# Kernel tuning notes

Hardware: AMD Instinct MI355X
Metric: run time of the kernel (lower is better)

The kernel has to match this reference:

```python
import jax, jax.numpy as jnp
import numpy as np

D_MODEL = 1024
NUM_HEADS = 16
ROPE_THETA = 10000.0
NEG_INF = -1.0e9  # matches torch masked_fill value


def _rope(x, cos, sin):
    # x: (B, H, S, d_k); cos/sin: (1, 1, S, d_k) with interleaved-pair layout
    x_even = x[..., ::2]
    x_odd = x[..., 1::2]
    x_rot = jnp.stack((-x_odd, x_even), axis=-1).reshape(x.shape)
    return x * cos + x_rot * sin


def setup_inputs() -> dict:
    key = jax.random.key(0)
    ks = jax.random.split(key, 5)
    B, S, D = 2, 2048, D_MODEL
    std = np.sqrt(2.0 / (D + D))
    return {
        "x": jax.random.normal(ks[0], (B, S, D), dtype=jnp.float32),
        "token_positions": jnp.arange(S, dtype=jnp.int32)[None, :],
        "Wq": jax.random.normal(ks[1], (D, D), dtype=jnp.float32) * std,
        "Wk": jax.random.normal(ks[2], (D, D), dtype=jnp.float32) * std,
        "Wv": jax.random.normal(ks[3], (D, D), dtype=jnp.float32) * std,
        "Wo": jax.random.normal(ks[4], (D, D), dtype=jnp.float32) * std,
    }


def reference(x, token_positions, Wq, Wk, Wv, Wo):
    B, S, D = x.shape
    H = NUM_HEADS
    dk = D // H

    def proj(W):
        return (x @ W.T).reshape(B, S, H, dk).transpose(0, 2, 1, 3)  # (B,H,S,dk)

    q, k, v = proj(Wq), proj(Wk), proj(Wv)

    # RoPE tables (interleaved repeat of each frequency)
    inv_freq = 1.0 / ROPE_THETA ** (jnp.arange(0, dk, 2, dtype=jnp.float32) / dk)
    angles = token_positions.astype(jnp.float32)[..., None] * inv_freq  # (1,S,dk/2)
    angles = jnp.repeat(angles, 2, axis=-1)  # (1,S,dk)
    cos = jnp.cos(angles)[:, None, :, :]  # (1,1,S,dk)
    sin = jnp.sin(angles)[:, None, :, :]
    q = _rope(q, cos, sin)
    k = _rope(k, cos, sin)

    scores = jnp.einsum("bhqd,bhkd->bhqk", q, k) / jnp.sqrt(jnp.float32(dk))
    causal = jnp.tril(jnp.ones((S, S), dtype=bool))
    scores = jnp.where(causal, scores, NEG_INF)
    attn = jax.nn.softmax(scores, axis=-1)
    out = jnp.einsum("bhqk,bhkd->bhqd", attn, v)
    out = out.transpose(0, 2, 1, 3).reshape(B, S, D)
    return out @ Wo.T
```

## Files before the change

kernel.cpp:

```cpp
#include <hip/hip_runtime.h>
#include <hip/hip_bf16.h>
#include <stdint.h>

typedef __bf16 bf16_t;
typedef __attribute__((ext_vector_type(8))) __bf16 bf16x8;
typedef __attribute__((ext_vector_type(4))) __bf16 bf16x4;
typedef __attribute__((ext_vector_type(2))) __bf16 bf16x2;
typedef __attribute__((ext_vector_type(4))) float f32x4;
typedef __attribute__((ext_vector_type(16))) float f32x16;
typedef __attribute__((ext_vector_type(4))) uint32_t u32x4;

#define S_LEN 2048
#define DMODEL 1024
#define NHEAD 16
#define DK 64
#define TENS_ELEMS 4194304

__device__ __forceinline__ void async_load16(const bf16_t* g, bf16_t* l) {
  __builtin_amdgcn_global_load_lds(
      (const __attribute__((address_space(1))) uint32_t*)(const void*)g,
      (__attribute__((address_space(3))) uint32_t*)(void*)l,
      16, 0, 0);
}

__device__ __forceinline__ uint32_t pack_bf16(float a, float b) {
  bf16x2 h; h[0] = (bf16_t)a; h[1] = (bf16_t)b;
  return __builtin_bit_cast(uint32_t, h);
}

__global__ __launch_bounds__(256) void cvt_all(const float* __restrict__ x,
                                               const float* __restrict__ w0,
                                               const float* __restrict__ w1,
                                               const float* __restrict__ w2,
                                               const float* __restrict__ w3,
                                               bf16_t* __restrict__ xb,
                                               bf16_t* __restrict__ wb) {
  int b = blockIdx.x;
  const float* s;
  bf16_t* d;
  int i;
  if (b < 4096) {
    s = x; d = xb; i = b * 256 + threadIdx.x;
  } else {
    int k = (b - 4096) >> 10, j = (b - 4096) & 1023;
    s = (k == 0) ? w0 : (k == 1) ? w1 : (k == 2) ? w2 : w3;
    d = wb + (size_t)k * 1048576;
    i = j * 256 + threadIdx.x;
  }
  float4 v = ((const float4*)s)[i];
  bf16x4 o;
  o.x = (bf16_t)v.x; o.y = (bf16_t)v.y; o.z = (bf16_t)v.z; o.w = (bf16_t)v.w;
  ((bf16x4*)d)[i] = o;
}

template <int MODE>
__global__ __launch_bounds__(256) void gemm_nt(const bf16_t* __restrict__ A,
                                               const bf16_t* __restrict__ Bw,
                                               bf16_t* __restrict__ Cb,
                                               float* __restrict__ Cf,
                                               const int* __restrict__ tok) {
  __shared__ bf16_t As[64 * 64];
  __shared__ bf16_t Bs[128 * 64];
  const int K = 1024;
  int tid = threadIdx.x;
  int lane = tid & 63, w = tid >> 6, lo = lane & 15, hi = lane >> 4;
  int m0 = blockIdx.y * 64, n0 = blockIdx.x * 128;
  const bf16_t* Bp = Bw + (size_t)blockIdx.z * 1048576;
  f32x4 acc[4][2] = {};
  for (int k0 = 0; k0 < K; k0 += 64) {
#pragma unroll
    for (int it = 0; it < 2; ++it) {
      int idx = it * 256 + tid;
      int row = idx >> 3, kc = (idx & 7) * 8;
      async_load16(A + (size_t)(m0 + row) * K + k0 + kc, &As[idx * 8]);
    }
#pragma unroll
    for (int it = 0; it < 4; ++it) {
      int idx = it * 256 + tid;
      int row = idx >> 3, kc = (idx & 7) * 8;
      async_load16(Bp + (size_t)(n0 + row) * K + k0 + kc, &Bs[idx * 8]);
    }
    __syncthreads();
#pragma unroll
    for (int ks = 0; ks < 2; ++ks) {
      bf16x8 af[4], bfr[2];
#pragma unroll
      for (int mi = 0; mi < 4; ++mi)
        af[mi] = *(const bf16x8*)&As[(mi * 16 + lo) * 64 + ks * 32 + hi * 8];
#pragma unroll
      for (int ni = 0; ni < 2; ++ni)
        bfr[ni] = *(const bf16x8*)&Bs[(w * 32 + ni * 16 + lo) * 64 + ks * 32 + hi * 8];
#pragma unroll
      for (int mi = 0; mi < 4; ++mi)
#pragma unroll
        for (int ni = 0; ni < 2; ++ni)
          acc[mi][ni] = __builtin_amdgcn_mfma_f32_16x16x32_bf16(af[mi], bfr[ni], acc[mi][ni], 0, 0, 0);
    }
    __syncthreads();
  }
#pragma unroll
  for (int mi = 0; mi < 4; ++mi) {
#pragma unroll
    for (int ni = 0; ni < 2; ++ni) {
      int col = n0 + w * 32 + ni * 16 + lo;
      int rb = m0 + mi * 16 + hi * 4;
      if (MODE == 0) {
        int h = col >> 6, d = col & 63;
        if (blockIdx.z == 2) {
          bf16_t* Vt = Cb + 3 * (size_t)TENS_ELEMS;
          int b = rb >> 11, s = rb & 2047;
          int bh2 = b * NHEAD + h;
          bf16x4 ov;
#pragma unroll
          for (int r = 0; r < 4; ++r) ov[r] = (bf16_t)acc[mi][ni][r];
          *(bf16x4*)(Vt + (((size_t)(bh2 * 32 + (s >> 6)) * 64 + d) * 64 + (s & 63))) = ov;
        } else {
          bf16_t* C = Cb + (size_t)blockIdx.z * TENS_ELEMS;
          float sc = (blockIdx.z == 0) ? 0.125f : 1.0f;
          int i2 = d >> 1;
          bool isOdd = (d & 1);
          float invf = __expf(-(float)i2 * 0.28782313662425572f);
#pragma unroll
          for (int r = 0; r < 4; ++r) {
            int row = rb + r;
            int b = row >> 11, s = row & 2047;
            float v = acc[mi][ni][r];
            float pv = __shfl_xor(v, 1);
            float sn, cs;
            sincosf((float)tok[s] * invf, &sn, &cs);
            float outv = isOdd ? (v * cs + pv * sn) : (v * cs - pv * sn);
            C[(((size_t)(b * NHEAD + h)) * S_LEN + s) * DK + d] = (bf16_t)(outv * sc);
          }
        }
      } else {
#pragma unroll
        for (int r = 0; r < 4; ++r) {
          int row = rb + r;
          Cf[(size_t)row * 1024 + col] = acc[mi][ni][r];
        }
      }
    }
  }
}

#define FIXM 12.0f
__global__ __launch_bounds__(256, 2) void attn_kernel(const bf16_t* __restrict__ Q,
                                                      const bf16_t* __restrict__ K,
                                                      const bf16_t* __restrict__ Vt,
                                                      bf16_t* __restrict__ O) {
  __shared__ float S_lds[3][32][66];
  int tid = threadIdx.x;
  int w = tid >> 6, lane = tid & 63;
  int lq = lane & 31, hi = lane >> 5;
  int g = blockIdx.x;
  int bh = (g & 7) * 4 + (g >> 8);
  int qp = (g >> 3) & 31;

  const bf16_t* Kb = K + (size_t)bh * S_LEN * DK;
  const bf16_t* Vb = Vt + (size_t)bh * DK * S_LEN;
  const bf16_t* kp = Kb + (size_t)lq * DK + hi * 8;
  int b_out = bh >> 4, h_out = bh & 15;

  for (int ph = 0; ph < 2; ++ph) {
    int qt = ph ? (63 - qp) : qp;
    int q0 = qt * 32;

    const bf16_t* Qp = Q + ((size_t)bh * S_LEN + q0 + lq) * DK + hi * 8;
    bf16x8 qf[4];
#pragma unroll
    for (int ks = 0; ks < 4; ++ks) qf[ks] = *(const bf16x8*)(Qp + ks * 16);

    f32x16 oa0 = {}, oa1 = {};
    float lsum = 0.f;

    int nT = (q0 + 95) >> 6;
    int tB = (nT * w) >> 2, tE = (nT * (w + 1)) >> 2;

    if (tB < tE) {
      bf16x8 kc[8];
      const bf16_t* kp0 = kp + (size_t)(tB * 64) * DK;
#pragma unroll
      for (int i = 0; i < 8; ++i)
        kc[i] = *(const bf16x8*)(kp0 + (size_t)(i >> 2) * 32 * DK + (i & 3) * 16);

      for (int t = tB; t < tE; ++t) {
        int kv0 = t * 64;
        bf16x8 vf[8];
        const bf16_t* vtile = Vb + (size_t)t * 4096 + 8 * hi;
#pragma unroll
        for (int sub = 0; sub < 2; ++sub)
#pragma unroll
          for (int u = 0; u < 4; ++u)
            vf[sub * 4 + u] = *(const bf16x8*)(vtile + (32 * sub + lq) * 64 + 16 * u);
        f32x16 s0 = {}, s1 = {};
        __builtin_amdgcn_s_setprio(1);
#pragma unroll
        for (int ks = 0; ks < 4; ++ks)
          s0 = __builtin_amdgcn_mfma_f32_32x32x16_bf16(kc[ks], qf[ks], s0, 0, 0, 0);
#pragma unroll
        for (int ks = 0; ks < 4; ++ks)
          s1 = __builtin_amdgcn_mfma_f32_32x32x16_bf16(kc[4 + ks], qf[ks], s1, 0, 0, 0);
        __builtin_amdgcn_s_setprio(0);
        bf16x8 kn[8];
        bool more = (t + 1 < tE);
        if (more) {
          const bf16_t* kpn = kp + (size_t)(kv0 + 64) * DK;
#pragma unroll
          for (int i = 0; i < 8; ++i)
            kn[i] = *(const bf16x8*)(kpn + (size_t)(i >> 2) * 32 * DK + (i & 3) * 16);
        }
        float p[32];
        bool needMask = (kv0 + 63 > q0);
#pragma unroll
        for (int r = 0; r < 16; ++r) {
          float v0 = s0[r] - FIXM, v1 = s1[r] - FIXM;
          if (needMask) {
            int kvr = kv0 + (r & 3) + 8 * (r >> 2) + 4 * hi;
            if (kvr > q0 + lq) v0 = -1e9f;
            if (kvr + 32 > q0 + lq) v1 = -1e9f;
          }
          p[r] = v0; p[16 + r] = v1;
        }
        float ts[16];
#pragma unroll
        for (int i = 0; i < 32; ++i) p[i] = __expf(p[i]);
#pragma unroll
        for (int i = 0; i < 16; ++i) ts[i] = p[i] + p[16 + i];
#pragma unroll
        for (int i = 0; i < 8; ++i) ts[i] += ts[8 + i];
#pragma unroll
        for (int i = 0; i < 4; ++i) ts[i] += ts[4 + i];
        float sum = (ts[0] + ts[1]) + (ts[2] + ts[3]);
        sum += __shfl_xor(sum, 32);
        lsum += sum;
        uint32_t pk[16], xk[16];
#pragma unroll
        for (int c = 0; c < 16; ++c) pk[c] = pack_bf16(p[2 * c], p[2 * c + 1]);
#pragma unroll
        for (int c = 0; c < 16; ++c) xk[c] = (uint32_t)__shfl_xor((int)pk[c], 32);
        __builtin_amdgcn_s_setprio(1);
#pragma unroll
        for (int tt = 0; tt < 2; ++tt)
#pragma unroll
          for (int j = 0; j < 2; ++j) {
            int c0 = 8 * tt + 4 * j;
            uint32_t b0 = hi ? xk[c0 + 2] : pk[c0];
            uint32_t b1 = hi ? xk[c0 + 3] : pk[c0 + 1];
            uint32_t b2 = hi ? pk[c0 + 2] : xk[c0];
            uint32_t b3 = hi ? pk[c0 + 3] : xk[c0 + 1];
            u32x4 bb = {b0, b1, b2, b3};
            bf16x8 pb = __builtin_bit_cast(bf16x8, bb);
            int u = 2 * tt + j;
            oa0 = __builtin_amdgcn_mfma_f32_32x32x16_bf16(vf[u], pb, oa0, 0, 0, 0);
            oa1 = __builtin_amdgcn_mfma_f32_32x32x16_bf16(vf[4 + u], pb, oa1, 0, 0, 0);
          }
        __builtin_amdgcn_s_setprio(0);
        if (more) {
#pragma unroll
          for (int i = 0; i < 8; ++i) kc[i] = kn[i];
        }
      }
    }

    if (w > 0) {
      float* Sp = &S_lds[w - 1][lq][0];
#pragma unroll
      for (int g2 = 0; g2 < 4; ++g2)
#pragma unroll
        for (int i = 0; i < 4; ++i) {
          Sp[8 * g2 + 4 * hi + i]      = oa0[4 * g2 + i];
          Sp[32 + 8 * g2 + 4 * hi + i] = oa1[4 * g2 + i];
        }
      if (hi == 0) { Sp[65] = lsum; }
    }
    __syncthreads();
    if (w == 0) {
      float lc = lsum + S_lds[0][lq][65] + S_lds[1][lq][65] + S_lds[2][lq][65];
      float inv = 1.0f / lc;
      bf16_t* Op = O + ((size_t)(b_out * S_LEN + q0 + lq)) * DMODEL + h_out * 64;
#pragma unroll
      for (int g2 = 0; g2 < 4; ++g2) {
        bf16x4 ov0, ov1;
#pragma unroll
        for (int i = 0; i < 4; ++i) {
          int c0 = 8 * g2 + 4 * hi + i;
          float v0 = oa0[4 * g2 + i] + S_lds[0][lq][c0]
                   + S_lds[1][lq][c0] + S_lds[2][lq][c0];
          float v1 = oa1[4 * g2 + i] + S_lds[0][lq][32 + c0]
                   + S_lds[1][lq][32 + c0] + S_lds[2][lq][32 + c0];
          ov0[i] = (bf16_t)(v0 * inv);
          ov1[i] = (bf16_t)(v1 * inv);
        }
        *(bf16x4*)(Op + 8 * g2 + 4 * hi) = ov0;
        *(bf16x4*)(Op + 32 + 8 * g2 + 4 * hi) = ov1;
      }
    }
    __syncthreads();
  }
}

extern "C" void kernel_launch(void* const* d_in, const int* in_sizes, int n_in,
                              void* d_out, int out_size, void* d_ws, size_t ws_size,
                              hipStream_t stream) {
  const float* x  = (const float*)d_in[0];
  const int* tok  = (const int*)d_in[1];
  const float* Wq = (const float*)d_in[2];
  const float* Wk = (const float*)d_in[3];
  const float* Wv = (const float*)d_in[4];
  const float* Wo = (const float*)d_in[5];
  float* out = (float*)d_out;

  bf16_t* xb  = (bf16_t*)d_ws;
  bf16_t* Wb  = xb + TENS_ELEMS;
  bf16_t* Qb  = Wb + TENS_ELEMS;
  bf16_t* Kb  = Qb + TENS_ELEMS;
  bf16_t* Vb  = Kb + TENS_ELEMS;
  bf16_t* Vtb = Vb + TENS_ELEMS;
  bf16_t* Ab  = Vtb + TENS_ELEMS;

  cvt_all<<<8192, 256, 0, stream>>>(x, Wq, Wk, Wv, Wo, xb, Wb);

  gemm_nt<0><<<dim3(8, 64, 3), 256, 0, stream>>>(xb, Wb, Qb, nullptr, tok);
  attn_kernel<<<1024, 256, 0, stream>>>(Qb, Kb, Vtb, Ab);
  gemm_nt<1><<<dim3(8, 64, 1), 256, 0, stream>>>(Ab, Wb + 3145728, nullptr, out, tok);
}
```

Measured before the change: 153.3 us.

## Fuse Q/K/V projections into one GEMM kernel sharing the A tile

Replaces the z-indexed QKV GEMM launch with a single kernel where each block computes Q, K and V outputs for the same row/column tile. The x tile is loaded once into shared memory and reused across all three weight matrices, which cuts global and LDS traffic for A. In exchange each block holds three times the accumulators and B-tile shared memory, and the grid is three times smaller (512 blocks at occupancy 1). That risks lower occupancy and less latency hiding on 256 CUs.

```diff
diff --git a/kernel.cpp b/kernel.cpp
--- a/kernel.cpp
+++ b/kernel.cpp
@@ -53,19 +53,104 @@
   ((bf16x4*)d)[i] = o;
 }
 
-template <int MODE>
-__global__ __launch_bounds__(256) void gemm_nt(const bf16_t* __restrict__ A,
-                                               const bf16_t* __restrict__ Bw,
-                                               bf16_t* __restrict__ Cb,
-                                               float* __restrict__ Cf,
-                                               const int* __restrict__ tok) {
+__global__ __launch_bounds__(256, 1) void gemm_qkv(const bf16_t* __restrict__ A,
+                                                   const bf16_t* __restrict__ Bw,
+                                                   bf16_t* __restrict__ Cb,
+                                                   const int* __restrict__ tok) {
+  __shared__ bf16_t As[64 * 64];
+  __shared__ bf16_t Bs[3][128 * 64];
+  const int K = 1024;
+  int tid = threadIdx.x;
+  int lane = tid & 63, w = tid >> 6, lo = lane & 15, hi = lane >> 4;
+  int m0 = blockIdx.y * 64, n0 = blockIdx.x * 128;
+  f32x4 acc[3][4][2] = {};
+  for (int k0 = 0; k0 < K; k0 += 64) {
+#pragma unroll
+    for (int it = 0; it < 2; ++it) {
+      int idx = it * 256 + tid;
+      int row = idx >> 3, kc = (idx & 7) * 8;
+      async_load16(A + (size_t)(m0 + row) * K + k0 + kc, &As[idx * 8]);
+    }
+#pragma unroll
+    for (int z = 0; z < 3; ++z)
+#pragma unroll
+      for (int it = 0; it < 4; ++it) {
+        int idx = it * 256 + tid;
+        int row = idx >> 3, kc = (idx & 7) * 8;
+        async_load16(Bw + (size_t)z * 1048576 + (size_t)(n0 + row) * K + k0 + kc,
+                     &Bs[z][idx * 8]);
+      }
+    __syncthreads();
+#pragma unroll
+    for (int ks = 0; ks < 2; ++ks) {
+      bf16x8 af[4];
+#pragma unroll
+      for (int mi = 0; mi < 4; ++mi)
+        af[mi] = *(const bf16x8*)&As[(mi * 16 + lo) * 64 + ks * 32 + hi * 8];
+#pragma unroll
+      for (int z = 0; z < 3; ++z) {
+        bf16x8 bfr[2];
+#pragma unroll
+        for (int ni = 0; ni < 2; ++ni)
+          bfr[ni] = *(const bf16x8*)&Bs[z][(w * 32 + ni * 16 + lo) * 64 + ks * 32 + hi * 8];
+#pragma unroll
+        for (int mi = 0; mi < 4; ++mi)
+#pragma unroll
+          for (int ni = 0; ni < 2; ++ni)
+            acc[z][mi][ni] = __builtin_amdgcn_mfma_f32_16x16x32_bf16(af[mi], bfr[ni], acc[z][mi][ni], 0, 0, 0);
+      }
+    }
+    __syncthreads();
+  }
+#pragma unroll
+  for (int z = 0; z < 3; ++z) {
+#pragma unroll
+    for (int mi = 0; mi < 4; ++mi) {
+#pragma unroll
+      for (int ni = 0; ni < 2; ++ni) {
+        int col = n0 + w * 32 + ni * 16 + lo;
+        int rb = m0 + mi * 16 + hi * 4;
+        int h = col >> 6, d = col & 63;
+        if (z == 2) {
+          bf16_t* Vt = Cb + 3 * (size_t)TENS_ELEMS;
+          int b = rb >> 11, s = rb & 2047;
+          int bh2 = b * NHEAD + h;
+          bf16x4 ov;
+#pragma unroll
+          for (int r = 0; r < 4; ++r) ov[r] = (bf16_t)acc[2][mi][ni][r];
+          *(bf16x4*)(Vt + (((size_t)(bh2 * 32 + (s >> 6)) * 64 + d) * 64 + (s & 63))) = ov;
+        } else {
+          bf16_t* C = Cb + (size_t)z * TENS_ELEMS;
+          float sc = (z == 0) ? 0.125f : 1.0f;
+          int i2 = d >> 1;
+          bool isOdd = (d & 1);
+          float invf = __expf(-(float)i2 * 0.28782313662425572f);
+#pragma unroll
+          for (int r = 0; r < 4; ++r) {
+            int row = rb + r;
+            int b = row >> 11, s = row & 2047;
+            float v = acc[z][mi][ni][r];
+            float pv = __shfl_xor(v, 1);
+            float sn, cs;
+            sincosf((float)tok[s] * invf, &sn, &cs);
+            float outv = isOdd ? (v * cs + pv * sn) : (v * cs - pv * sn);
+            C[(((size_t)(b * NHEAD + h)) * S_LEN + s) * DK + d] = (bf16_t)(outv * sc);
+          }
+        }
+      }
+    }
+  }
+}
+
+__global__ __launch_bounds__(256) void gemm_out(const bf16_t* __restrict__ A,
+                                                const bf16_t* __restrict__ Bw,
+                                                float* __restrict__ Cf) {
   __shared__ bf16_t As[64 * 64];
   __shared__ bf16_t Bs[128 * 64];
   const int K = 1024;
   int tid = threadIdx.x;
   int lane = tid & 63, w = tid >> 6, lo = lane & 15, hi = lane >> 4;
   int m0 = blockIdx.y * 64, n0 = blockIdx.x * 128;
-  const bf16_t* Bp = Bw + (size_t)blockIdx.z * 1048576;
   f32x4 acc[4][2] = {};
   for (int k0 = 0; k0 < K; k0 += 64) {
 #pragma unroll
@@ -78,7 +163,7 @@
     for (int it = 0; it < 4; ++it) {
       int idx = it * 256 + tid;
       int row = idx >> 3, kc = (idx & 7) * 8;
-      async_load16(Bp + (size_t)(n0 + row) * K + k0 + kc, &Bs[idx * 8]);
+      async_load16(Bw + (size_t)(n0 + row) * K + k0 + kc, &Bs[idx * 8]);
     }
     __syncthreads();
 #pragma unroll
@@ -99,48 +184,15 @@
     __syncthreads();
   }
 #pragma unroll
-  for (int mi = 0; mi < 4; ++mi) {
+  for (int mi = 0; mi < 4; ++mi)
 #pragma unroll
     for (int ni = 0; ni < 2; ++ni) {
       int col = n0 + w * 32 + ni * 16 + lo;
       int rb = m0 + mi * 16 + hi * 4;
-      if (MODE == 0) {
-        int h = col >> 6, d = col & 63;
-        if (blockIdx.z == 2) {
-          bf16_t* Vt = Cb + 3 * (size_t)TENS_ELEMS;
-          int b = rb >> 11, s = rb & 2047;
-          int bh2 = b * NHEAD + h;
-          bf16x4 ov;
-#pragma unroll
-          for (int r = 0; r < 4; ++r) ov[r] = (bf16_t)acc[mi][ni][r];
-          *(bf16x4*)(Vt + (((size_t)(bh2 * 32 + (s >> 6)) * 64 + d) * 64 + (s & 63))) = ov;
-        } else {
-          bf16_t* C = Cb + (size_t)blockIdx.z * TENS_ELEMS;
-          float sc = (blockIdx.z == 0) ? 0.125f : 1.0f;
-          int i2 = d >> 1;
-          bool isOdd = (d & 1);
-          float invf = __expf(-(float)i2 * 0.28782313662425572f);
-#pragma unroll
-          for (int r = 0; r < 4; ++r) {
-            int row = rb + r;
-            int b = row >> 11, s = row & 2047;
-            float v = acc[mi][ni][r];
-            float pv = __shfl_xor(v, 1);
-            float sn, cs;
-            sincosf((float)tok[s] * invf, &sn, &cs);
-            float outv = isOdd ? (v * cs + pv * sn) : (v * cs - pv * sn);
-            C[(((size_t)(b * NHEAD + h)) * S_LEN + s) * DK + d] = (bf16_t)(outv * sc);
-          }
-        }
-      } else {
-#pragma unroll
-        for (int r = 0; r < 4; ++r) {
-          int row = rb + r;
-          Cf[(size_t)row * 1024 + col] = acc[mi][ni][r];
-        }
-      }
-    }
-  }
+#pragma unroll
+      for (int r = 0; r < 4; ++r)
+        Cf[(size_t)(rb + r) * 1024 + col] = acc[mi][ni][r];
+    }
 }
 
 #define FIXM 12.0f
@@ -320,7 +372,7 @@
 
   cvt_all<<<8192, 256, 0, stream>>>(x, Wq, Wk, Wv, Wo, xb, Wb);
 
-  gemm_nt<0><<<dim3(8, 64, 3), 256, 0, stream>>>(xb, Wb, Qb, nullptr, tok);
+  gemm_qkv<<<dim3(8, 64), 256, 0, stream>>>(xb, Wb, Qb, tok);
   attn_kernel<<<1024, 256, 0, stream>>>(Qb, Kb, Vtb, Ab);
-  gemm_nt<1><<<dim3(8, 64, 1), 256, 0, stream>>>(Ab, Wb + 3145728, nullptr, out, tok);
-}
+  gemm_out<<<dim3(8, 64), 256, 0, stream>>>(Ab, Wb + 3145728, out);
+}
```

Result: slower. 432.6 us (+182.3%).
